# Kernel optimization log

Hardware: AMD Instinct MI355X
Metric: run time of the kernel (lower is better)

## Reference

```python
import jax, jax.numpy as jnp
import numpy as np

B, T, D_ENC, H, NUM_CLASSES = 256, 256, 512, 512, 96


def setup_inputs() -> dict:
    key = jax.random.key(0)
    ks = jax.random.split(key, 12)
    s = lambda k, shp, fan: jax.random.normal(k, shp, jnp.float32) / np.sqrt(fan)
    return {
        "prev_h": jax.random.normal(ks[0], (B, H), jnp.float32),
        "prev_c": jax.random.normal(ks[1], (B, H), jnp.float32),
        "batch_H": jax.random.normal(ks[2], (B, T, D_ENC), jnp.float32),
        "char_onehots": jax.random.uniform(ks[3], (B, NUM_CLASSES), jnp.float32),
        # i2h: Dense(D_ENC -> H, no bias); h2h: Dense(H -> H, bias); score: Dense(H -> 1, no bias)
        "Wi2h": s(ks[4], (D_ENC, H), D_ENC),
        "Wh2h": s(ks[5], (H, H), H),
        "bh2h": jnp.zeros((H,), jnp.float32),
        "Wscore": s(ks[6], (H, 1), H),
        # LSTMCell: input dim = D_ENC + NUM_CLASSES, gates [i, f, g, o]
        "Wk": s(ks[7], (D_ENC + NUM_CLASSES, 4 * H), D_ENC + NUM_CLASSES),
        "Uk": s(ks[8], (H, 4 * H), H),
        "bk": jnp.zeros((4 * H,), jnp.float32),
    }


def reference(prev_h, prev_c, batch_H, char_onehots, Wi2h, Wh2h, bh2h, Wscore, Wk, Uk, bk):
    # Bahdanau additive attention
    bH_proj = jnp.einsum('btd,dh->bth', batch_H, Wi2h)          # [B,T,H]
    h_proj = (prev_h @ Wh2h + bh2h)[:, None, :]                  # [B,1,H]
    e = jnp.tanh(bH_proj + h_proj) @ Wscore                      # [B,T,1]
    alpha = jax.nn.softmax(e, axis=1)                            # [B,T,1]
    context = jnp.einsum('bt,btd->bd', alpha[..., 0], batch_H)   # [B,D_enc]
    # LSTM cell step on [context ; char_onehots]
    x = jnp.concatenate([context, char_onehots], axis=1)         # [B, D_enc+num_classes]
    z = x @ Wk + prev_h @ Uk + bk                                # [B, 4H]
    i, f, g, o = jnp.split(z, 4, axis=1)
    c_new = jax.nn.sigmoid(f) * prev_c + jax.nn.sigmoid(i) * jnp.tanh(g)
    h_new = jax.nn.sigmoid(o) * jnp.tanh(c_new)
    return h_new, c_new, alpha
```

## Files before the change

kernel.cpp:

```cpp
#include <hip/hip_runtime.h>

typedef __bf16 bf16_t;
typedef bf16_t bf16x8 __attribute__((ext_vector_type(8)));
typedef unsigned short ushort8_t __attribute__((ext_vector_type(8)));
typedef unsigned short ushort4_t __attribute__((ext_vector_type(4)));
typedef float f32x4 __attribute__((ext_vector_type(4)));

__device__ __forceinline__ unsigned short f2bf(float f) {
    __bf16 h = (__bf16)f;
    return __builtin_bit_cast(unsigned short, h);
}
__device__ __forceinline__ float fast_tanh(float x) {
    float e2 = __expf(2.f * x);
    return 1.f - 2.f / (e2 + 1.f);
}
__device__ __forceinline__ float fast_sig(float x) {
    return 1.f / (1.f + __expf(-x));
}

__global__ void k0_wt2(const float* __restrict__ Wi2h, const float* __restrict__ Wh2h,
                       unsigned short* __restrict__ Wt, unsigned short* __restrict__ Wht) {
    __shared__ float tile[32][33];
    const float* W = blockIdx.z ? Wh2h : Wi2h;
    unsigned short* O = blockIdx.z ? Wht : Wt;
    int tx = threadIdx.x, ty = threadIdx.y;
    int bx = blockIdx.x, by = blockIdx.y;
#pragma unroll
    for (int j = 0; j < 4; ++j) {
        int r = by * 32 + ty + j * 8;
        int c = bx * 32 + tx;
        tile[ty + j * 8][tx] = W[r * 512 + c];
    }
    __syncthreads();
#pragma unroll
    for (int j = 0; j < 4; ++j) {
        int h = bx * 32 + ty + j * 8;
        int d = by * 32 + tx;
        O[h * 512 + d] = f2bf(tile[tx][ty + j * 8]);
    }
}

__global__ void k1x_conv(const float* __restrict__ src, unsigned short* __restrict__ dst) {
    int i = blockIdx.x * 256 + threadIdx.x;
    float4 f = ((const float4*)src)[i];
    ushort4_t u;
    u[0] = f2bf(f.x); u[1] = f2bf(f.y); u[2] = f2bf(f.z); u[3] = f2bf(f.w);
    ((ushort4_t*)dst)[i] = u;
}

__global__ void k1m_hproj(const unsigned short* __restrict__ ph_bf,
                          const unsigned short* __restrict__ Wht,
                          const float* __restrict__ bh2h,
                          float* __restrict__ h_proj) {
    int tid = threadIdx.x;
    int wave = tid >> 6, lane = tid & 63;
    int l15 = lane & 15, g = lane >> 4;
    int h0 = blockIdx.x * 64 + wave * 16;
    int m0 = blockIdx.y * 32;

    f32x4 acc[2];
    acc[0] = (f32x4){0.f, 0.f, 0.f, 0.f};
    acc[1] = (f32x4){0.f, 0.f, 0.f, 0.f};

    const unsigned short* abase = ph_bf + (size_t)(m0 + l15) * 512 + g * 8;
    const unsigned short* bbase = Wht + (size_t)(h0 + l15) * 512 + g * 8;
#pragma unroll
    for (int j = 0; j < 16; ++j) {
        bf16x8 bf = __builtin_bit_cast(bf16x8, *(const ushort8_t*)(bbase + j * 32));
        bf16x8 a0 = __builtin_bit_cast(bf16x8, *(const ushort8_t*)(abase + j * 32));
        bf16x8 a1 = __builtin_bit_cast(bf16x8, *(const ushort8_t*)(abase + 16 * 512 + j * 32));
        acc[0] = __builtin_amdgcn_mfma_f32_16x16x32_bf16(a0, bf, acc[0], 0, 0, 0);
        acc[1] = __builtin_amdgcn_mfma_f32_16x16x32_bf16(a1, bf, acc[1], 0, 0, 0);
    }
    int h = h0 + l15;
    float bias = bh2h[h];
#pragma unroll
    for (int mf = 0; mf < 2; ++mf)
#pragma unroll
        for (int r = 0; r < 4; ++r)
            h_proj[(size_t)(m0 + mf * 16 + g * 4 + r) * 512 + h] = acc[mf][r] + bias;
}

__launch_bounds__(256, 4)
__global__ void k2_scores(const float* __restrict__ batch_H,
                          const unsigned short* __restrict__ Wt,
                          const float* __restrict__ h_proj,
                          const float* __restrict__ Wscore,
                          float* __restrict__ e_part) {
    __shared__ __align__(16) unsigned short Alds[8192];
    __shared__ __align__(16) unsigned short Blds[8192];
    __shared__ float hp_s[128];
    __shared__ float wsc_s[128];
    __shared__ float e_red[4][64];

    int tid = threadIdx.x;
    int wg = (blockIdx.x & 7) * 256 + (blockIdx.x >> 3);
    int mt = wg >> 2, nt = wg & 3;
    int m0 = mt * 128, n0 = nt * 128;
    int b  = m0 >> 8;

    if (tid < 128) hp_s[tid] = h_proj[(size_t)b * 512 + n0 + tid];
    else           wsc_s[tid - 128] = Wscore[n0 + tid - 128];

    int wave = tid >> 6;
    int lane = tid & 63;
    int wr = wave >> 1;
    int wc = wave & 1;
    int l15 = lane & 15, g = lane >> 4;
    int bchunk = ((lane & 7) ^ (lane >> 3)) << 3;
    int brow_l = lane >> 3;

    f32x4 acc[4][4];
#pragma unroll
    for (int mf = 0; mf < 4; ++mf)
#pragma unroll
        for (int nf = 0; nf < 4; ++nf)
            acc[mf][nf] = (f32x4){0.f, 0.f, 0.f, 0.f};

    for (int ks = 0; ks < 8; ++ks) {
        __syncthreads();
        int kbase = ks * 64;
#pragma unroll
        for (int i = 0; i < 4; ++i) {
            int q = wave * 4 + i;
            int row = q * 8 + brow_l;
            const unsigned short* gsrc = Wt + (size_t)(n0 + row) * 512 + kbase + bchunk;
            __builtin_amdgcn_global_load_lds(
                (const __attribute__((address_space(1))) void*)gsrc,
                (__attribute__((address_space(3))) void*)&Blds[q * 512], 16, 0, 0);
        }
        float4 av[8];
#pragma unroll
        for (int j = 0; j < 8; ++j) {
            int idx = j * 256 + tid;
            int r = idx >> 4, c4 = idx & 15;
            av[j] = *(const float4*)(batch_H + (size_t)(m0 + r) * 512 + kbase + c4 * 4);
        }
#pragma unroll
        for (int j = 0; j < 8; ++j) {
            int idx = j * 256 + tid;
            int r = idx >> 4, c4 = idx & 15;
            ushort4_t u;
            u[0] = f2bf(av[j].x); u[1] = f2bf(av[j].y);
            u[2] = f2bf(av[j].z); u[3] = f2bf(av[j].w);
            int boff = r * 128 + ((((c4 >> 1) ^ (r & 7)) << 4) | ((c4 & 1) << 3));
            *(ushort4_t*)((char*)Alds + boff) = u;
        }
        __syncthreads();
#pragma unroll
        for (int kk = 0; kk < 2; ++kk) {
            bf16x8 af[4], bfr[4];
#pragma unroll
            for (int mf = 0; mf < 4; ++mf) {
                int row = wr * 64 + mf * 16 + l15;
                int boff = row * 128 + ((((kk * 4 + g) ^ (l15 & 7))) << 4);
                af[mf] = __builtin_bit_cast(bf16x8, *(const ushort8_t*)((char*)Alds + boff));
            }
#pragma unroll
            for (int nf = 0; nf < 4; ++nf) {
                int row = wc * 64 + nf * 16 + l15;
                int boff = row * 128 + ((((kk * 4 + g) ^ (l15 & 7))) << 4);
                bfr[nf] = __builtin_bit_cast(bf16x8, *(const ushort8_t*)((char*)Blds + boff));
            }
#pragma unroll
            for (int nf = 0; nf < 4; ++nf)
#pragma unroll
                for (int mf = 0; mf < 4; ++mf)
                    acc[mf][nf] = __builtin_amdgcn_mfma_f32_16x16x32_bf16(
                        af[mf], bfr[nf], acc[mf][nf], 0, 0, 0);
        }
    }

    float s[4][4];
#pragma unroll
    for (int mf = 0; mf < 4; ++mf)
#pragma unroll
        for (int r = 0; r < 4; ++r) s[mf][r] = 0.f;

#pragma unroll
    for (int nf = 0; nf < 4; ++nf) {
        int nl = wc * 64 + nf * 16 + l15;
        float hpv = hp_s[nl], wv = wsc_s[nl];
#pragma unroll
        for (int mf = 0; mf < 4; ++mf)
#pragma unroll
            for (int r = 0; r < 4; ++r)
                s[mf][r] += wv * fast_tanh(acc[mf][nf][r] + hpv);
    }
#pragma unroll
    for (int mf = 0; mf < 4; ++mf)
#pragma unroll
        for (int r = 0; r < 4; ++r) {
            float v = s[mf][r];
            v += __shfl_xor(v, 1);
            v += __shfl_xor(v, 2);
            v += __shfl_xor(v, 4);
            v += __shfl_xor(v, 8);
            s[mf][r] = v;
        }
    if (l15 == 0) {
#pragma unroll
        for (int mf = 0; mf < 4; ++mf)
#pragma unroll
            for (int r = 0; r < 4; ++r)
                e_red[wave][mf * 16 + g * 4 + r] = s[mf][r];
    }
    __syncthreads();
    if (tid < 128) {
        int wrr = tid >> 6, i64 = tid & 63;
        float v = e_red[wrr * 2 + 0][i64] + e_red[wrr * 2 + 1][i64];
        e_part[(size_t)nt * 65536 + m0 + tid] = v;
    }
}

__global__ void k3_softmax(const float* __restrict__ e_part, float* __restrict__ alpha_out) {
    __shared__ float red[4];
    int b = blockIdx.x, tid = threadIdx.x;
    int m = b * 256 + tid;
    float v = e_part[m] + e_part[65536 + m] + e_part[131072 + m] + e_part[196608 + m];
    float mx = v;
#pragma unroll
    for (int off = 32; off; off >>= 1) mx = fmaxf(mx, __shfl_xor(mx, off));
    if ((tid & 63) == 0) red[tid >> 6] = mx;
    __syncthreads();
    mx = fmaxf(fmaxf(red[0], red[1]), fmaxf(red[2], red[3]));
    float p = __expf(v - mx);
    __syncthreads();
    float sum = p;
#pragma unroll
    for (int off = 32; off; off >>= 1) sum += __shfl_xor(sum, off);
    if ((tid & 63) == 0) red[tid >> 6] = sum;
    __syncthreads();
    sum = red[0] + red[1] + red[2] + red[3];
    alpha_out[b * 256 + tid] = p / sum;
}

__global__ void k4_context(const float* __restrict__ batch_H, const float* __restrict__ alpha,
                           float* __restrict__ context) {
    __shared__ float al[256];
    int b = blockIdx.y, dc = blockIdx.x, tid = threadIdx.x;
    al[tid] = alpha[b * 256 + tid];
    __syncthreads();
    int d = dc * 256 + tid;
    const float* bh = batch_H + (size_t)b * 256 * 512 + d;
    float acc = 0.f;
#pragma unroll 4
    for (int t = 0; t < 256; ++t)
        acc += al[t] * bh[(size_t)t * 512];
    context[b * 512 + d] = acc;
}

__global__ void k5t_wzt(const float* __restrict__ Wk, const float* __restrict__ Uk,
                        unsigned short* __restrict__ Wzt) {
    __shared__ float tile[32][33];
    int tx = threadIdx.x, ty = threadIdx.y;
    int bx = blockIdx.x;
    int by = blockIdx.y;
#pragma unroll
    for (int j = 0; j < 4; ++j) {
        int k = bx * 32 + ty + j * 8;
        int c = by * 32 + tx;
        float v = (k < 608) ? Wk[(size_t)k * 2048 + c] : Uk[(size_t)(k - 608) * 2048 + c];
        tile[ty + j * 8][tx] = v;
    }
    __syncthreads();
#pragma unroll
    for (int j = 0; j < 4; ++j) {
        int n = by * 32 + ty + j * 8;
        int k = bx * 32 + tx;
        Wzt[(size_t)n * 1120 + k] = f2bf(tile[tx][ty + j * 8]);
    }
}

__global__ void k5x_build(const float* __restrict__ context, const float* __restrict__ onehots,
                          const float* __restrict__ prev_h, unsigned short* __restrict__ xb) {
    int b = blockIdx.x, tid = threadIdx.x;
    for (int k = tid; k < 1120; k += 256) {
        float v;
        if (k < 512)      v = context[b * 512 + k];
        else if (k < 608) v = onehots[b * 96 + k - 512];
        else              v = prev_h[b * 512 + k - 608];
        xb[(size_t)b * 1120 + k] = f2bf(v);
    }
}

__launch_bounds__(256)
__global__ void k5m_fused(const unsigned short* __restrict__ xb,
                          const unsigned short* __restrict__ Wzt,
                          const float* __restrict__ bk,
                          const float* __restrict__ prev_c,
                          float* __restrict__ out) {
    __shared__ __align__(16) unsigned short Axs[32 * 232];

    int tid  = threadIdx.x;
    int wave = tid >> 6;
    int lane = tid & 63;
    int l15  = lane & 15;
    int g    = lane >> 4;
    int b0   = blockIdx.y * 32;
    int h0   = blockIdx.x * 64 + wave * 16;

    f32x4 acc[2][4];
#pragma unroll
    for (int mf = 0; mf < 2; ++mf)
#pragma unroll
        for (int gt = 0; gt < 4; ++gt)
            acc[mf][gt] = (f32x4){0.f, 0.f, 0.f, 0.f};

    const unsigned short* wbase = Wzt + (size_t)(h0 + l15) * 1120;

    for (int ks = 0; ks < 5; ++ks) {
        if (ks) __syncthreads();
        int kbase = ks * 224;
        for (int i = tid; i < 896; i += 256) {
            int row = i / 28;
            int c8  = (i % 28) * 8;
            *(ushort8_t*)(&Axs[row * 232 + c8]) =
                *(const ushort8_t*)(&xb[(size_t)(b0 + row) * 1120 + kbase + c8]);
        }
        __syncthreads();

        bf16x8 bcur[4], bnxt[4];
#pragma unroll
        for (int gt = 0; gt < 4; ++gt)
            bcur[gt] = __builtin_bit_cast(bf16x8,
                *(const ushort8_t*)(wbase + (size_t)gt * 512 * 1120 + kbase + g * 8));

#pragma unroll
        for (int kb = 0; kb < 7; ++kb) {
            if (kb < 6) {
                int kg = kbase + (kb + 1) * 32 + g * 8;
#pragma unroll
                for (int gt = 0; gt < 4; ++gt)
                    bnxt[gt] = __builtin_bit_cast(bf16x8,
                        *(const ushort8_t*)(wbase + (size_t)gt * 512 * 1120 + kg));
            }
            bf16x8 afrag[2];
#pragma unroll
            for (int mf = 0; mf < 2; ++mf)
                afrag[mf] = __builtin_bit_cast(bf16x8,
                    *(const ushort8_t*)(&Axs[(mf * 16 + l15) * 232 + kb * 32 + g * 8]));
#pragma unroll
            for (int gt = 0; gt < 4; ++gt)
#pragma unroll
                for (int mf = 0; mf < 2; ++mf)
                    acc[mf][gt] = __builtin_amdgcn_mfma_f32_16x16x32_bf16(
                        afrag[mf], bcur[gt], acc[mf][gt], 0, 0, 0);
#pragma unroll
            for (int gt = 0; gt < 4; ++gt) bcur[gt] = bnxt[gt];
        }
    }

    int h = h0 + l15;
    float bi = bk[h], bfv = bk[512 + h], bg = bk[1024 + h], bo = bk[1536 + h];
#pragma unroll
    for (int mf = 0; mf < 2; ++mf)
#pragma unroll
        for (int r = 0; r < 4; ++r) {
            int m = b0 + mf * 16 + g * 4 + r;
            float zi = acc[mf][0][r] + bi;
            float zf = acc[mf][1][r] + bfv;
            float zg = acc[mf][2][r] + bg;
            float zo = acc[mf][3][r] + bo;
            float c  = fast_sig(zf) * prev_c[m * 512 + h] + fast_sig(zi) * fast_tanh(zg);
            float hn = fast_sig(zo) * fast_tanh(c);
            out[m * 512 + h]          = hn;
            out[131072 + m * 512 + h] = c;
        }
}

extern "C" void kernel_launch(void* const* d_in, const int* in_sizes, int n_in,
                              void* d_out, int out_size, void* d_ws, size_t ws_size,
                              hipStream_t stream) {
    (void)in_sizes; (void)n_in; (void)out_size; (void)ws_size;
    const float* prev_h  = (const float*)d_in[0];
    const float* prev_c  = (const float*)d_in[1];
    const float* batch_H = (const float*)d_in[2];
    const float* onehots = (const float*)d_in[3];
    const float* Wi2h    = (const float*)d_in[4];
    const float* Wh2h    = (const float*)d_in[5];
    const float* bh2h    = (const float*)d_in[6];
    const float* Wscore  = (const float*)d_in[7];
    const float* Wk      = (const float*)d_in[8];
    const float* Uk      = (const float*)d_in[9];
    const float* bk      = (const float*)d_in[10];
    float* out = (float*)d_out;
    float* alpha = out + 262144;

    char* ws = (char*)d_ws;
    unsigned short* Wt     = (unsigned short*)(ws + 0);
    unsigned short* Wht    = (unsigned short*)(ws + 524288);
    unsigned short* ph_bf  = (unsigned short*)(ws + 1048576);
    float*          h_proj = (float*)(ws + 1310720);
    float*          e_part = (float*)(ws + 1835008);
    unsigned short* Wzt    = (unsigned short*)(ws + 0);
    unsigned short* xb     = (unsigned short*)(ws + 4587520);
    float*          context= (float*)(ws + 5160960);

    k0_wt2    <<<dim3(16, 16, 2), dim3(32, 8), 0, stream>>>(Wi2h, Wh2h, Wt, Wht);
    k1x_conv  <<<128, 256, 0, stream>>>(prev_h, ph_bf);
    k1m_hproj <<<dim3(8, 8), 256, 0, stream>>>(ph_bf, Wht, bh2h, h_proj);
    k2_scores <<<2048, 256, 0, stream>>>(batch_H, Wt, h_proj, Wscore, e_part);
    k3_softmax<<<256, 256, 0, stream>>>(e_part, alpha);
    k4_context<<<dim3(2, 256), 256, 0, stream>>>(batch_H, alpha, context);
    k5t_wzt   <<<dim3(35, 64), dim3(32, 8), 0, stream>>>(Wk, Uk, Wzt);
    k5x_build <<<256, 256, 0, stream>>>(context, onehots, prev_h, xb);
    k5m_fused <<<dim3(8, 8), 256, 0, stream>>>(xb, Wzt, bk, prev_c, out);
}
```

Measured before the change: 166.5 us.

## Double-buffer LDS tiles in score GEMM to overlap global loads with MFMA

The k2_scores main loop now uses two LDS buffers for A and B. The next K-slice's global loads (global_load_lds for weights, float4 loads for batch_H) are issued before the MFMA work on the current slice, and the bf16 conversion into the alternate buffer happens afterwards, so each step needs one barrier instead of two. s_setprio is raised around the MFMA block. The cost is double the LDS footprint and a launch-bounds hint lowered from 4 to 2 blocks per CU, which reduces occupancy.

```diff
diff --git a/kernel.cpp b/kernel.cpp
--- a/kernel.cpp
+++ b/kernel.cpp
@@ -81,14 +81,14 @@
             h_proj[(size_t)(m0 + mf * 16 + g * 4 + r) * 512 + h] = acc[mf][r] + bias;
 }
 
-__launch_bounds__(256, 4)
+__launch_bounds__(256, 2)
 __global__ void k2_scores(const float* __restrict__ batch_H,
                           const unsigned short* __restrict__ Wt,
                           const float* __restrict__ h_proj,
                           const float* __restrict__ Wscore,
                           float* __restrict__ e_part) {
-    __shared__ __align__(16) unsigned short Alds[8192];
-    __shared__ __align__(16) unsigned short Blds[8192];
+    __shared__ __align__(16) unsigned short Alds[2][8192];
+    __shared__ __align__(16) unsigned short Blds[2][8192];
     __shared__ float hp_s[128];
     __shared__ float wsc_s[128];
     __shared__ float e_red[4][64];
@@ -109,6 +109,8 @@
     int l15 = lane & 15, g = lane >> 4;
     int bchunk = ((lane & 7) ^ (lane >> 3)) << 3;
     int brow_l = lane >> 3;
+    int ar  = tid >> 4;
+    int ac4 = tid & 15;
 
     f32x4 acc[4][4];
 #pragma unroll
@@ -117,36 +119,48 @@
         for (int nf = 0; nf < 4; ++nf)
             acc[mf][nf] = (f32x4){0.f, 0.f, 0.f, 0.f};
 
-    for (int ks = 0; ks < 8; ++ks) {
-        __syncthreads();
-        int kbase = ks * 64;
-#pragma unroll
-        for (int i = 0; i < 4; ++i) {
-            int q = wave * 4 + i;
-            int row = q * 8 + brow_l;
-            const unsigned short* gsrc = Wt + (size_t)(n0 + row) * 512 + kbase + bchunk;
-            __builtin_amdgcn_global_load_lds(
-                (const __attribute__((address_space(1))) void*)gsrc,
-                (__attribute__((address_space(3))) void*)&Blds[q * 512], 16, 0, 0);
-        }
-        float4 av[8];
-#pragma unroll
-        for (int j = 0; j < 8; ++j) {
-            int idx = j * 256 + tid;
-            int r = idx >> 4, c4 = idx & 15;
-            av[j] = *(const float4*)(batch_H + (size_t)(m0 + r) * 512 + kbase + c4 * 4);
-        }
-#pragma unroll
-        for (int j = 0; j < 8; ++j) {
-            int idx = j * 256 + tid;
-            int r = idx >> 4, c4 = idx & 15;
-            ushort4_t u;
-            u[0] = f2bf(av[j].x); u[1] = f2bf(av[j].y);
-            u[2] = f2bf(av[j].z); u[3] = f2bf(av[j].w);
-            int boff = r * 128 + ((((c4 >> 1) ^ (r & 7)) << 4) | ((c4 & 1) << 3));
-            *(ushort4_t*)((char*)Alds + boff) = u;
-        }
-        __syncthreads();
+    float4 av[8];
+
+#pragma unroll
+    for (int i = 0; i < 4; ++i) {
+        int q = wave * 4 + i, row = q * 8 + brow_l;
+        const unsigned short* gsrc = Wt + (size_t)(n0 + row) * 512 + bchunk;
+        __builtin_amdgcn_global_load_lds(
+            (const __attribute__((address_space(1))) void*)gsrc,
+            (__attribute__((address_space(3))) void*)&Blds[0][q * 512], 16, 0, 0);
+    }
+#pragma unroll
+    for (int j = 0; j < 8; ++j)
+        av[j] = *(const float4*)(batch_H + (size_t)(m0 + j * 16 + ar) * 512 + ac4 * 4);
+#pragma unroll
+    for (int j = 0; j < 8; ++j) {
+        int r = j * 16 + ar;
+        ushort4_t u;
+        u[0] = f2bf(av[j].x); u[1] = f2bf(av[j].y);
+        u[2] = f2bf(av[j].z); u[3] = f2bf(av[j].w);
+        int boff = r * 128 + ((((ac4 >> 1) ^ (r & 7)) << 4) | ((ac4 & 1) << 3));
+        *(ushort4_t*)((char*)&Alds[0][0] + boff) = u;
+    }
+    __syncthreads();
+
+#pragma unroll
+    for (int t = 0; t < 8; ++t) {
+        const int cur = t & 1;
+        if (t < 7) {
+#pragma unroll
+            for (int i = 0; i < 4; ++i) {
+                int q = wave * 4 + i, row = q * 8 + brow_l;
+                const unsigned short* gsrc =
+                    Wt + (size_t)(n0 + row) * 512 + (t + 1) * 64 + bchunk;
+                __builtin_amdgcn_global_load_lds(
+                    (const __attribute__((address_space(1))) void*)gsrc,
+                    (__attribute__((address_space(3))) void*)&Blds[cur ^ 1][q * 512], 16, 0, 0);
+            }
+#pragma unroll
+            for (int j = 0; j < 8; ++j)
+                av[j] = *(const float4*)(batch_H +
+                    (size_t)(m0 + j * 16 + ar) * 512 + (t + 1) * 64 + ac4 * 4);
+        }
 #pragma unroll
         for (int kk = 0; kk < 2; ++kk) {
             bf16x8 af[4], bfr[4];
@@ -154,21 +168,37 @@
             for (int mf = 0; mf < 4; ++mf) {
                 int row = wr * 64 + mf * 16 + l15;
                 int boff = row * 128 + ((((kk * 4 + g) ^ (l15 & 7))) << 4);
-                af[mf] = __builtin_bit_cast(bf16x8, *(const ushort8_t*)((char*)Alds + boff));
+                af[mf] = __builtin_bit_cast(bf16x8,
+                    *(const ushort8_t*)((char*)&Alds[cur][0] + boff));
             }
 #pragma unroll
             for (int nf = 0; nf < 4; ++nf) {
                 int row = wc * 64 + nf * 16 + l15;
                 int boff = row * 128 + ((((kk * 4 + g) ^ (l15 & 7))) << 4);
-                bfr[nf] = __builtin_bit_cast(bf16x8, *(const ushort8_t*)((char*)Blds + boff));
+                bfr[nf] = __builtin_bit_cast(bf16x8,
+                    *(const ushort8_t*)((char*)&Blds[cur][0] + boff));
             }
+            __builtin_amdgcn_s_setprio(1);
 #pragma unroll
             for (int nf = 0; nf < 4; ++nf)
 #pragma unroll
                 for (int mf = 0; mf < 4; ++mf)
                     acc[mf][nf] = __builtin_amdgcn_mfma_f32_16x16x32_bf16(
                         af[mf], bfr[nf], acc[mf][nf], 0, 0, 0);
-        }
+            __builtin_amdgcn_s_setprio(0);
+        }
+        if (t < 7) {
+#pragma unroll
+            for (int j = 0; j < 8; ++j) {
+                int r = j * 16 + ar;
+                ushort4_t u;
+                u[0] = f2bf(av[j].x); u[1] = f2bf(av[j].y);
+                u[2] = f2bf(av[j].z); u[3] = f2bf(av[j].w);
+                int boff = r * 128 + ((((ac4 >> 1) ^ (r & 7)) << 4) | ((ac4 & 1) << 3));
+                *(ushort4_t*)((char*)&Alds[cur ^ 1][0] + boff) = u;
+            }
+        }
+        __syncthreads();
     }
 
     float s[4][4];
```

Measured after the change: 152.4 us. 1.09x faster.

## Triple-buffer k2_scores LDS tiles with register-prefetched A and async B loads

Applied to the files above, without the earlier changes.

Rewrites the k2_scores main loop from eight 64-wide K steps, each with two block barriers, into a 16-step pipeline of 32-wide K tiles held in a three-slot LDS ring. B tiles are staged via global_load_lds two tiles ahead, and A tiles are loaded into registers two tiles ahead and converted to bf16 one step ahead, so one barrier per step overlaps memory traffic with MFMA work. It also uses s_setprio around the MFMA block and lowers launch bounds from 4 to 2 blocks per CU. This adds LDS use and register pressure and lowers occupancy. Correctness depends on a bare s_waitcnt lgkmcnt covering the global_load_lds writes before the barrier.

```diff
diff --git a/kernel.cpp b/kernel.cpp
--- a/kernel.cpp
+++ b/kernel.cpp
@@ -81,14 +81,14 @@
             h_proj[(size_t)(m0 + mf * 16 + g * 4 + r) * 512 + h] = acc[mf][r] + bias;
 }
 
-__launch_bounds__(256, 4)
+__launch_bounds__(256, 2)
 __global__ void k2_scores(const float* __restrict__ batch_H,
                           const unsigned short* __restrict__ Wt,
                           const float* __restrict__ h_proj,
                           const float* __restrict__ Wscore,
                           float* __restrict__ e_part) {
-    __shared__ __align__(16) unsigned short Alds[8192];
-    __shared__ __align__(16) unsigned short Blds[8192];
+    __shared__ __align__(16) char Asl[3][8192];
+    __shared__ __align__(16) char Bsl[3][8192];
     __shared__ float hp_s[128];
     __shared__ float wsc_s[128];
     __shared__ float e_red[4][64];
@@ -104,11 +104,12 @@
 
     int wave = tid >> 6;
     int lane = tid & 63;
-    int wr = wave >> 1;
-    int wc = wave & 1;
+    int wr = wave >> 1, wc = wave & 1;
     int l15 = lane & 15, g = lane >> 4;
-    int bchunk = ((lane & 7) ^ (lane >> 3)) << 3;
-    int brow_l = lane >> 3;
+    int brow0 = lane >> 2;
+    int bs    = lane & 3;
+    int ar8 = tid >> 3;
+    int ac4 = tid & 7;
 
     f32x4 acc[4][4];
 #pragma unroll
@@ -117,59 +118,96 @@
         for (int nf = 0; nf < 4; ++nf)
             acc[mf][nf] = (f32x4){0.f, 0.f, 0.f, 0.f};
 
-    for (int ks = 0; ks < 8; ++ks) {
-        __syncthreads();
-        int kbase = ks * 64;
-#pragma unroll
-        for (int i = 0; i < 4; ++i) {
-            int q = wave * 4 + i;
-            int row = q * 8 + brow_l;
-            const unsigned short* gsrc = Wt + (size_t)(n0 + row) * 512 + kbase + bchunk;
-            __builtin_amdgcn_global_load_lds(
-                (const __attribute__((address_space(1))) void*)gsrc,
-                (__attribute__((address_space(3))) void*)&Blds[q * 512], 16, 0, 0);
-        }
-        float4 av[8];
-#pragma unroll
-        for (int j = 0; j < 8; ++j) {
-            int idx = j * 256 + tid;
-            int r = idx >> 4, c4 = idx & 15;
-            av[j] = *(const float4*)(batch_H + (size_t)(m0 + r) * 512 + kbase + c4 * 4);
-        }
-#pragma unroll
-        for (int j = 0; j < 8; ++j) {
-            int idx = j * 256 + tid;
-            int r = idx >> 4, c4 = idx & 15;
-            ushort4_t u;
-            u[0] = f2bf(av[j].x); u[1] = f2bf(av[j].y);
-            u[2] = f2bf(av[j].z); u[3] = f2bf(av[j].w);
-            int boff = r * 128 + ((((c4 >> 1) ^ (r & 7)) << 4) | ((c4 & 1) << 3));
-            *(ushort4_t*)((char*)Alds + boff) = u;
-        }
-        __syncthreads();
-#pragma unroll
-        for (int kk = 0; kk < 2; ++kk) {
+    float4 av0[4], av1[4];
+
+#define STAGE_B(tile, slot)                                                              \
+    {                                                                                    \
+        _Pragma("unroll")                                                                \
+        for (int i_ = 0; i_ < 2; ++i_) {                                                 \
+            int rowbase_ = (wave * 2 + i_) * 16;                                         \
+            int row_ = rowbase_ + brow0;                                                 \
+            int chunk_ = bs ^ ((row_ >> 1) & 3);                                         \
+            const unsigned short* src_ = Wt + (size_t)(n0 + row_) * 512 + (tile) * 32 + chunk_ * 8; \
+            __builtin_amdgcn_global_load_lds(                                            \
+                (const __attribute__((address_space(1))) void*)src_,                     \
+                (__attribute__((address_space(3))) void*)(&Bsl[slot][rowbase_ * 64]), 16, 0, 0); \
+        }                                                                                \
+    }
+
+#define LOAD_A(avreg, tile)                                                              \
+    {                                                                                    \
+        _Pragma("unroll")                                                                \
+        for (int p_ = 0; p_ < 4; ++p_)                                                   \
+            avreg[p_] = *(const float4*)(batch_H + (size_t)(m0 + p_ * 32 + ar8) * 512 + (tile) * 32 + ac4 * 4); \
+    }
+
+#define WRITE_A(avreg, slot)                                                             \
+    {                                                                                    \
+        _Pragma("unroll")                                                                \
+        for (int p_ = 0; p_ < 4; ++p_) {                                                 \
+            int r_ = p_ * 32 + ar8;                                                      \
+            ushort4_t u_;                                                                \
+            u_[0] = f2bf(avreg[p_].x); u_[1] = f2bf(avreg[p_].y);                        \
+            u_[2] = f2bf(avreg[p_].z); u_[3] = f2bf(avreg[p_].w);                        \
+            int off_ = r_ * 64 + ((((ac4 >> 1) ^ ((r_ >> 1) & 3))) << 4) + ((ac4 & 1) << 3); \
+            *(ushort4_t*)(&Asl[slot][off_]) = u_;                                        \
+        }                                                                                \
+    }
+
+    STAGE_B(0, 0)
+    STAGE_B(1, 1)
+    __builtin_amdgcn_sched_barrier(0);
+    LOAD_A(av0, 0)
+    LOAD_A(av1, 1)
+    WRITE_A(av0, 0)
+    asm volatile("s_waitcnt lgkmcnt(0)" ::: "memory");
+    __builtin_amdgcn_s_barrier();
+    __builtin_amdgcn_sched_barrier(0);
+
+#pragma unroll
+    for (int t = 0; t < 16; ++t) {
+        const int slotC = t % 3, slotW = (t + 1) % 3, slotL = (t + 2) % 3;
+        if (t < 15) {
+            if (t & 1) { WRITE_A(av0, slotW) }
+            else       { WRITE_A(av1, slotW) }
+        }
+        if (t < 14) {
+            STAGE_B(t + 2, slotL)
+            __builtin_amdgcn_sched_barrier(0);
+            if (t & 1) { LOAD_A(av1, t + 2) }
+            else       { LOAD_A(av0, t + 2) }
+        }
+        {
             bf16x8 af[4], bfr[4];
 #pragma unroll
             for (int mf = 0; mf < 4; ++mf) {
                 int row = wr * 64 + mf * 16 + l15;
-                int boff = row * 128 + ((((kk * 4 + g) ^ (l15 & 7))) << 4);
-                af[mf] = __builtin_bit_cast(bf16x8, *(const ushort8_t*)((char*)Alds + boff));
+                af[mf] = __builtin_bit_cast(bf16x8,
+                    *(const ushort8_t*)(&Asl[slotC][row * 64 + (((g ^ ((row >> 1) & 3))) << 4)]));
             }
 #pragma unroll
             for (int nf = 0; nf < 4; ++nf) {
                 int row = wc * 64 + nf * 16 + l15;
-                int boff = row * 128 + ((((kk * 4 + g) ^ (l15 & 7))) << 4);
-                bfr[nf] = __builtin_bit_cast(bf16x8, *(const ushort8_t*)((char*)Blds + boff));
+                bfr[nf] = __builtin_bit_cast(bf16x8,
+                    *(const ushort8_t*)(&Bsl[slotC][row * 64 + (((g ^ ((row >> 1) & 3))) << 4)]));
             }
+            __builtin_amdgcn_s_setprio(1);
 #pragma unroll
             for (int nf = 0; nf < 4; ++nf)
 #pragma unroll
                 for (int mf = 0; mf < 4; ++mf)
                     acc[mf][nf] = __builtin_amdgcn_mfma_f32_16x16x32_bf16(
                         af[mf], bfr[nf], acc[mf][nf], 0, 0, 0);
-        }
-    }
+            __builtin_amdgcn_s_setprio(0);
+        }
+        asm volatile("s_waitcnt lgkmcnt(0)" ::: "memory");
+        __builtin_amdgcn_sched_barrier(0);
+        __builtin_amdgcn_s_barrier();
+        __builtin_amdgcn_sched_barrier(0);
+    }
+#undef STAGE_B
+#undef LOAD_A
+#undef WRITE_A
 
     float s[4][4];
 #pragma unroll
```

New measurement: 153.2 us. 1.09x faster.

## Fuse softmax with context, fold bf16 conversions into GEMM loaders

Applied to the files above, without the earlier changes.

Merges softmax and context reduction into one kernel per batch row. It also removes the separate prev_h conversion and x-build kernels by converting fp32 to bf16 inside the h_proj and LSTM GEMM A-loaders. Separately, k2's launch bounds are relaxed from 4 to 3 waves per SIMD. The aim is fewer launches and fewer intermediate buffer round trips, at the cost of less parallelism in the context kernel (256 blocks instead of 512) and repeated fp32 loads in the GEMMs.

```diff
diff --git a/kernel.cpp b/kernel.cpp
--- a/kernel.cpp
+++ b/kernel.cpp
@@ -16,6 +16,12 @@
 }
 __device__ __forceinline__ float fast_sig(float x) {
     return 1.f / (1.f + __expf(-x));
+}
+__device__ __forceinline__ ushort8_t cvt8(float4 f0, float4 f1) {
+    ushort8_t u;
+    u[0] = f2bf(f0.x); u[1] = f2bf(f0.y); u[2] = f2bf(f0.z); u[3] = f2bf(f0.w);
+    u[4] = f2bf(f1.x); u[5] = f2bf(f1.y); u[6] = f2bf(f1.z); u[7] = f2bf(f1.w);
+    return u;
 }
 
 __global__ void k0_wt2(const float* __restrict__ Wi2h, const float* __restrict__ Wh2h,
@@ -40,15 +46,7 @@
     }
 }
 
-__global__ void k1x_conv(const float* __restrict__ src, unsigned short* __restrict__ dst) {
-    int i = blockIdx.x * 256 + threadIdx.x;
-    float4 f = ((const float4*)src)[i];
-    ushort4_t u;
-    u[0] = f2bf(f.x); u[1] = f2bf(f.y); u[2] = f2bf(f.z); u[3] = f2bf(f.w);
-    ((ushort4_t*)dst)[i] = u;
-}
-
-__global__ void k1m_hproj(const unsigned short* __restrict__ ph_bf,
+__global__ void k1m_hproj(const float* __restrict__ prev_h,
                           const unsigned short* __restrict__ Wht,
                           const float* __restrict__ bh2h,
                           float* __restrict__ h_proj) {
@@ -62,13 +60,17 @@
     acc[0] = (f32x4){0.f, 0.f, 0.f, 0.f};
     acc[1] = (f32x4){0.f, 0.f, 0.f, 0.f};
 
-    const unsigned short* abase = ph_bf + (size_t)(m0 + l15) * 512 + g * 8;
+    const float* abase = prev_h + (size_t)(m0 + l15) * 512 + g * 8;
     const unsigned short* bbase = Wht + (size_t)(h0 + l15) * 512 + g * 8;
 #pragma unroll
     for (int j = 0; j < 16; ++j) {
         bf16x8 bf = __builtin_bit_cast(bf16x8, *(const ushort8_t*)(bbase + j * 32));
-        bf16x8 a0 = __builtin_bit_cast(bf16x8, *(const ushort8_t*)(abase + j * 32));
-        bf16x8 a1 = __builtin_bit_cast(bf16x8, *(const ushort8_t*)(abase + 16 * 512 + j * 32));
+        float4 f0 = *(const float4*)(abase + j * 32);
+        float4 f1 = *(const float4*)(abase + j * 32 + 4);
+        bf16x8 a0 = __builtin_bit_cast(bf16x8, cvt8(f0, f1));
+        float4 f2 = *(const float4*)(abase + 16 * 512 + j * 32);
+        float4 f3 = *(const float4*)(abase + 16 * 512 + j * 32 + 4);
+        bf16x8 a1 = __builtin_bit_cast(bf16x8, cvt8(f2, f3));
         acc[0] = __builtin_amdgcn_mfma_f32_16x16x32_bf16(a0, bf, acc[0], 0, 0, 0);
         acc[1] = __builtin_amdgcn_mfma_f32_16x16x32_bf16(a1, bf, acc[1], 0, 0, 0);
     }
@@ -81,7 +83,7 @@
             h_proj[(size_t)(m0 + mf * 16 + g * 4 + r) * 512 + h] = acc[mf][r] + bias;
 }
 
-__launch_bounds__(256, 4)
+__launch_bounds__(256, 3)
 __global__ void k2_scores(const float* __restrict__ batch_H,
                           const unsigned short* __restrict__ Wt,
                           const float* __restrict__ h_proj,
@@ -213,8 +215,10 @@
     }
 }
 
-__global__ void k3_softmax(const float* __restrict__ e_part, float* __restrict__ alpha_out) {
+__global__ void k3k4_fused(const float* __restrict__ e_part, const float* __restrict__ batch_H,
+                           float* __restrict__ alpha_out, float* __restrict__ context) {
     __shared__ float red[4];
+    __shared__ float al[256];
     int b = blockIdx.x, tid = threadIdx.x;
     int m = b * 256 + tid;
     float v = e_part[m] + e_part[65536 + m] + e_part[131072 + m] + e_part[196608 + m];
@@ -232,22 +236,20 @@
     if ((tid & 63) == 0) red[tid >> 6] = sum;
     __syncthreads();
     sum = red[0] + red[1] + red[2] + red[3];
-    alpha_out[b * 256 + tid] = p / sum;
-}
-
-__global__ void k4_context(const float* __restrict__ batch_H, const float* __restrict__ alpha,
-                           float* __restrict__ context) {
-    __shared__ float al[256];
-    int b = blockIdx.y, dc = blockIdx.x, tid = threadIdx.x;
-    al[tid] = alpha[b * 256 + tid];
-    __syncthreads();
-    int d = dc * 256 + tid;
-    const float* bh = batch_H + (size_t)b * 256 * 512 + d;
-    float acc = 0.f;
+    float a = p / sum;
+    alpha_out[b * 256 + tid] = a;
+    al[tid] = a;
+    __syncthreads();
+    const float* bh = batch_H + (size_t)b * 131072;
+    float ac0 = 0.f, ac1 = 0.f;
 #pragma unroll 4
-    for (int t = 0; t < 256; ++t)
-        acc += al[t] * bh[(size_t)t * 512];
-    context[b * 512 + d] = acc;
+    for (int t = 0; t < 256; ++t) {
+        float av = al[t];
+        ac0 += av * bh[t * 512 + tid];
+        ac1 += av * bh[t * 512 + tid + 256];
+    }
+    context[b * 512 + tid]       = ac0;
+    context[b * 512 + tid + 256] = ac1;
 }
 
 __global__ void k5t_wzt(const float* __restrict__ Wk, const float* __restrict__ Uk,
@@ -272,20 +274,9 @@
     }
 }
 
-__global__ void k5x_build(const float* __restrict__ context, const float* __restrict__ onehots,
-                          const float* __restrict__ prev_h, unsigned short* __restrict__ xb) {
-    int b = blockIdx.x, tid = threadIdx.x;
-    for (int k = tid; k < 1120; k += 256) {
-        float v;
-        if (k < 512)      v = context[b * 512 + k];
-        else if (k < 608) v = onehots[b * 96 + k - 512];
-        else              v = prev_h[b * 512 + k - 608];
-        xb[(size_t)b * 1120 + k] = f2bf(v);
-    }
-}
-
 __launch_bounds__(256)
-__global__ void k5m_fused(const unsigned short* __restrict__ xb,
+__global__ void k5m_fused(const float* __restrict__ context, const float* __restrict__ onehots,
+                          const float* __restrict__ prev_h,
                           const unsigned short* __restrict__ Wzt,
                           const float* __restrict__ bk,
                           const float* __restrict__ prev_c,
@@ -315,8 +306,20 @@
         for (int i = tid; i < 896; i += 256) {
             int row = i / 28;
             int c8  = (i % 28) * 8;
-            *(ushort8_t*)(&Axs[row * 232 + c8]) =
-                *(const ushort8_t*)(&xb[(size_t)(b0 + row) * 1120 + kbase + c8]);
+            int gk  = kbase + c8;
+            int gb  = b0 + row;
+            ushort8_t u;
+            if (gk < 512) {
+                const float* s = context + (size_t)gb * 512 + gk;
+                u = cvt8(*(const float4*)s, *(const float4*)(s + 4));
+            } else if (gk < 608) {
+                const float* s = onehots + (size_t)gb * 96 + (gk - 512);
+                u = cvt8(*(const float4*)s, *(const float4*)(s + 4));
+            } else {
+                const float* s = prev_h + (size_t)gb * 512 + (gk - 608);
+                u = cvt8(*(const float4*)s, *(const float4*)(s + 4));
+            }
+            *(ushort8_t*)(&Axs[row * 232 + c8]) = u;
         }
         __syncthreads();
 
@@ -390,20 +393,15 @@
     char* ws = (char*)d_ws;
     unsigned short* Wt     = (unsigned short*)(ws + 0);
     unsigned short* Wht    = (unsigned short*)(ws + 524288);
-    unsigned short* ph_bf  = (unsigned short*)(ws + 1048576);
-    float*          h_proj = (float*)(ws + 1310720);
-    float*          e_part = (float*)(ws + 1835008);
+    float*          h_proj = (float*)(ws + 1048576);
+    float*          e_part = (float*)(ws + 1572864);
     unsigned short* Wzt    = (unsigned short*)(ws + 0);
-    unsigned short* xb     = (unsigned short*)(ws + 4587520);
-    float*          context= (float*)(ws + 5160960);
+    float*          context= (float*)(ws + 4587520);
 
     k0_wt2    <<<dim3(16, 16, 2), dim3(32, 8), 0, stream>>>(Wi2h, Wh2h, Wt, Wht);
-    k1x_conv  <<<128, 256, 0, stream>>>(prev_h, ph_bf);
-    k1m_hproj <<<dim3(8, 8), 256, 0, stream>>>(ph_bf, Wht, bh2h, h_proj);
+    k1m_hproj <<<dim3(8, 8), 256, 0, stream>>>(prev_h, Wht, bh2h, h_proj);
     k2_scores <<<2048, 256, 0, stream>>>(batch_H, Wt, h_proj, Wscore, e_part);
-    k3_softmax<<<256, 256, 0, stream>>>(e_part, alpha);
-    k4_context<<<dim3(2, 256), 256, 0, stream>>>(batch_H, alpha, context);
+    k3k4_fused<<<256, 256, 0, stream>>>(e_part, batch_H, alpha, context);
     k5t_wzt   <<<dim3(35, 64), dim3(32, 8), 0, stream>>>(Wk, Uk, Wzt);
-    k5x_build <<<256, 256, 0, stream>>>(context, onehots, prev_h, xb);
-    k5m_fused <<<dim3(8, 8), 256, 0, stream>>>(xb, Wzt, bk, prev_c, out);
-}
+    k5m_fused <<<dim3(8, 8), 256, 0, stream>>>(context, onehots, prev_h, Wzt, bk, prev_c, out);
+}
```

Result: faster. 147.2 us (-11.6%).
